# Performance work log

Hardware: AMD Instinct MI355X
Metric: run time of the kernel (lower is better)

The kernel has to match this reference:

```python
import jax, jax.numpy as jnp
import numpy as np

DIM = 1024
NUM_HEADS = 16
HEAD_DIM = DIM // NUM_HEADS
TGT_LEN = 4096


def setup_inputs() -> dict:
    key = jax.random.key(0)
    k1, k2, k3 = jax.random.split(key, 3)
    x = jax.random.normal(k1, (TGT_LEN, DIM), dtype=jnp.float32)
    W_in = jax.random.normal(k2, (3 * DIM, DIM), dtype=jnp.float32) * (DIM ** -0.5)
    W_out = jax.random.normal(k3, (DIM, DIM), dtype=jnp.float32) * (DIM ** -0.5)
    return {"x": x, "W_in": W_in, "W_out": W_out, "tgt_len": TGT_LEN}


def reference(x, W_in, W_out, tgt_len):
    # QKV projection (torch Linear: y = x @ W^T)
    qkv = x @ W_in.T  # [T, 3*dim]
    q, k, v = jnp.split(qkv, 3, axis=-1)
    # [T, dim] -> [H, T, hd]
    q = q.reshape(tgt_len, NUM_HEADS, HEAD_DIM).transpose(1, 0, 2)
    k = k.reshape(tgt_len, NUM_HEADS, HEAD_DIM).transpose(1, 0, 2)
    v = v.reshape(tgt_len, NUM_HEADS, HEAD_DIM).transpose(1, 0, 2)
    scaling = HEAD_DIM ** -0.5
    scores = jnp.einsum('htd,hsd->hts', q, k) * scaling  # [H, T, T]
    # joint softmax over the full (T, T) matrix per head (NOT row-wise)
    maxes = jnp.max(scores, axis=(1, 2), keepdims=True)
    x_exp = jnp.exp(scores - maxes)
    probs = x_exp / jnp.sum(x_exp, axis=(1, 2), keepdims=True)
    attn = jnp.einsum('hts,hsd->htd', probs, v)  # [H, T, hd]
    attn = attn.transpose(1, 0, 2).reshape(tgt_len, DIM)
    return attn @ W_out.T
```

## Files before the change

kernel.cpp:

```cpp
#include <hip/hip_runtime.h>

#define TLEN 4096
#define DIM 1024
#define NHEAD 16
#define HDIM 64
#define QKV_COLS (3 * DIM)
#define QSCALE 0.1803368801111244f
#define NCHUNK 2
#define SCHUNK (TLEN / NCHUNK)
#define TB 256

typedef __attribute__((ext_vector_type(8))) short short8;
typedef __attribute__((ext_vector_type(4))) float f32x4;

struct alignas(8) s4 { short v[4]; };

__device__ float g_Lsum[NHEAD];
__device__ float g_recipL[NHEAD];

__global__ void zeroL() {
    if (threadIdx.x < NHEAD) g_Lsum[threadIdx.x] = 0.0f;
}
__global__ void recipL() {
    if (threadIdx.x < NHEAD) g_recipL[threadIdx.x] = 1.0f / g_Lsum[threadIdx.x];
}

__device__ __forceinline__ unsigned bf16_rtne_bits(float x) {
    unsigned u = __float_as_uint(x);
    return (u + 0x7fffu + ((u >> 16) & 1u)) >> 16;
}

__device__ __forceinline__ void cp16(const short* g, short* l) {
    __builtin_amdgcn_global_load_lds(
        (const __attribute__((address_space(1))) unsigned int*)g,
        (__attribute__((address_space(3))) unsigned int*)l,
        16, 0, 0);
}

__device__ __forceinline__ short8 mk8(unsigned a, unsigned b, unsigned c, unsigned d) {
    union { unsigned u[4]; short8 s; } t;
    t.u[0] = a; t.u[1] = b; t.u[2] = c; t.u[3] = d;
    return t.s;
}

__global__ __launch_bounds__(256) void conv_bf16(
    const float* __restrict__ src, short* __restrict__ dst, int n4)
{
    int i = blockIdx.x * 256 + threadIdx.x;
    if (i < n4) {
        float4 v = ((const float4*)src)[i];
        s4 o;
        o.v[0] = (short)bf16_rtne_bits(v.x);
        o.v[1] = (short)bf16_rtne_bits(v.y);
        o.v[2] = (short)bf16_rtne_bits(v.z);
        o.v[3] = (short)bf16_rtne_bits(v.w);
        ((s4*)dst)[i] = o;
    }
}

__global__ __launch_bounds__(256) void conv_wout(
    const float* __restrict__ src, short* __restrict__ dst)
{
    int i = blockIdx.x * 256 + threadIdx.x;
    float s = g_recipL[(i & 255) >> 4];
    float4 v = ((const float4*)src)[i];
    s4 o;
    o.v[0] = (short)bf16_rtne_bits(v.x * s);
    o.v[1] = (short)bf16_rtne_bits(v.y * s);
    o.v[2] = (short)bf16_rtne_bits(v.z * s);
    o.v[3] = (short)bf16_rtne_bits(v.w * s);
    ((s4*)dst)[i] = o;
}

__global__ __launch_bounds__(256) void combine(
    const short* __restrict__ p0, const short* __restrict__ p1,
    short* __restrict__ dst, int n4)
{
    int i = blockIdx.x * 256 + threadIdx.x;
    if (i < n4) {
        s4 a = ((const s4*)p0)[i];
        s4 b = ((const s4*)p1)[i];
        s4 o;
#pragma unroll
        for (int m = 0; m < 4; ++m) {
            float fa = __uint_as_float(((unsigned)(unsigned short)a.v[m]) << 16);
            float fb = __uint_as_float(((unsigned)(unsigned short)b.v[m]) << 16);
            o.v[m] = (short)bf16_rtne_bits(fa + fb);
        }
        ((s4*)dst)[i] = o;
    }
}

template <bool QKV_MODE>
__global__ __launch_bounds__(256) void gemm_bt(
    const short* __restrict__ A, const short* __restrict__ B,
    void* __restrict__ Cout, short* __restrict__ Vout, int M, int N, int K)
{
    __shared__ __align__(16) short As[128][32];
    __shared__ __align__(16) short Bs[128][32];
    const int tid  = threadIdx.x;
    const int wv   = tid >> 6, lane = tid & 63;
    const int fr   = lane & 15, quad = lane >> 4;
    const int wm   = (wv >> 1) * 64, wn = (wv & 1) * 64;
    const int m0 = blockIdx.x * 128, n0 = blockIdx.y * 128;

    f32x4 acc[4][4] = {};

    for (int k0 = 0; k0 < K; k0 += 32) {
        __syncthreads();
#pragma unroll
        for (int c = tid; c < 512; c += 256) {
            int row = c >> 2, col = (c & 3) * 8;
            cp16(A + (size_t)(m0 + row) * K + k0 + col, &As[row][col]);
            cp16(B + (size_t)(n0 + row) * K + k0 + col, &Bs[row][col]);
        }
        __syncthreads();

        short8 af[4], bfr[4];
#pragma unroll
        for (int i = 0; i < 4; ++i) {
            af[i]  = *(const short8*)&As[wm + i * 16 + fr][quad * 8];
            bfr[i] = *(const short8*)&Bs[wn + i * 16 + fr][quad * 8];
        }
#pragma unroll
        for (int i = 0; i < 4; ++i)
#pragma unroll
            for (int j = 0; j < 4; ++j)
                acc[i][j] = __builtin_amdgcn_mfma_f32_16x16x32_bf16(af[i], bfr[j], acc[i][j], 0, 0, 0);
    }

    if (QKV_MODE && n0 >= 2 * DIM) {
#pragma unroll
        for (int i = 0; i < 4; ++i)
#pragma unroll
            for (int j = 0; j < 4; ++j) {
                int n = n0 - 2 * DIM + wn + j * 16 + fr;
                int m = m0 + wm + i * 16 + quad * 4;
                unsigned u0 = bf16_rtne_bits(acc[i][j][0]);
                unsigned u1 = bf16_rtne_bits(acc[i][j][1]);
                unsigned u2 = bf16_rtne_bits(acc[i][j][2]);
                unsigned u3 = bf16_rtne_bits(acc[i][j][3]);
                uint2 pk;
                pk.x = u0 | (u1 << 16);
                pk.y = u2 | (u3 << 16);
                *(uint2*)(Vout + (size_t)n * TLEN + m) = pk;
            }
    } else if (QKV_MODE) {
        const float sc = (n0 < DIM) ? QSCALE : 1.0f;
#pragma unroll
        for (int i = 0; i < 4; ++i)
#pragma unroll
            for (int j = 0; j < 4; ++j)
#pragma unroll
                for (int r = 0; r < 4; ++r) {
                    size_t off = (size_t)(m0 + wm + i * 16 + quad * 4 + r) * N + n0 + wn + j * 16 + fr;
                    ((short*)Cout)[off] = (short)bf16_rtne_bits(acc[i][j][r] * sc);
                }
    } else {
#pragma unroll
        for (int i = 0; i < 4; ++i)
#pragma unroll
            for (int j = 0; j < 4; ++j)
#pragma unroll
                for (int r = 0; r < 4; ++r) {
                    size_t off = (size_t)(m0 + wm + i * 16 + quad * 4 + r) * N + n0 + wn + j * 16 + fr;
                    ((float*)Cout)[off] = acc[i][j][r];
                }
    }
}

__global__ __launch_bounds__(256, 2) void attn_mfma(
    const short* __restrict__ qkvb, const short* __restrict__ vtb,
    short* __restrict__ part)
{
    __shared__ __align__(16) short Ks[64][72];
    __shared__ __align__(16) short Vt[64][72];
    __shared__ float red[256];

    const int tid = threadIdx.x;
    const int t0 = blockIdx.x * TB;
    const int h  = blockIdx.y;
    const int chunk = blockIdx.z;
    const int srow = tid >> 2;
    const int sch  = (tid & 3) * 16;
    const int wv   = tid >> 6;
    const int lane = tid & 63;
    const int fr   = lane & 15;
    const int quad = lane >> 4;
    const int tb   = wv * 64;

    short8 qf[4][2];
#pragma unroll
    for (int jt = 0; jt < 4; ++jt) {
        const short* qsrc = qkvb + (size_t)(t0 + tb + jt * 16 + fr) * QKV_COLS + h * HDIM + quad * 8;
        qf[jt][0] = *(const short8*)qsrc;
        qf[jt][1] = *(const short8*)(qsrc + 32);
    }

    short8 ones;
#pragma unroll
    for (int m = 0; m < 8; ++m) ones[m] = (short)0x3F80;

    f32x4 oaccT[4][4] = {};
    f32x4 racc[4] = {};

    const int s_begin = chunk * SCHUNK;
    const short* kbase = qkvb + DIM + h * HDIM + sch;
    const short* vbase = vtb + (size_t)(h * HDIM + srow) * TLEN + sch;

    uint4 kA, kB, vA, vB;
    {
        const short* ks = kbase + (size_t)(s_begin + srow) * QKV_COLS;
        kA = *(const uint4*)ks;  kB = *(const uint4*)(ks + 8);
        const short* vs = vbase + s_begin;
        vA = *(const uint4*)vs;  vB = *(const uint4*)(vs + 8);
    }

    for (int it = 0; it < SCHUNK / 64; ++it) {
        *(uint4*)&Ks[srow][sch]     = kA;
        *(uint4*)&Ks[srow][sch + 8] = kB;
        *(uint4*)&Vt[srow][sch]     = vA;
        *(uint4*)&Vt[srow][sch + 8] = vB;
        __syncthreads();

        if (it + 1 < SCHUNK / 64) {
            const int s0n = s_begin + (it + 1) * 64;
            const short* ks = kbase + (size_t)(s0n + srow) * QKV_COLS;
            kA = *(const uint4*)ks;  kB = *(const uint4*)(ks + 8);
            const short* vs = vbase + s0n;
            vA = *(const uint4*)vs;  vB = *(const uint4*)(vs + 8);
        }

        short8 kf[4][2], vf[4][2];
#pragma unroll
        for (int i = 0; i < 4; ++i) {
            kf[i][0] = *(const short8*)&Ks[i * 16 + fr][quad * 8];
            kf[i][1] = *(const short8*)&Ks[i * 16 + fr][32 + quad * 8];
            vf[i][0] = *(const short8*)&Vt[i * 16 + fr][quad * 8];
            vf[i][1] = *(const short8*)&Vt[i * 16 + fr][32 + quad * 8];
        }

#pragma unroll
        for (int jt = 0; jt < 4; ++jt) {
            unsigned w0[4], w1[4];
#pragma unroll
            for (int i = 0; i < 4; ++i) {
                f32x4 acc = {};
                acc = __builtin_amdgcn_mfma_f32_16x16x32_bf16(kf[i][0], qf[jt][0], acc, 0, 0, 0);
                acc = __builtin_amdgcn_mfma_f32_16x16x32_bf16(kf[i][1], qf[jt][1], acc, 0, 0, 0);
                unsigned u0 = __float_as_uint(__builtin_amdgcn_exp2f(acc[0]));
                unsigned u1 = __float_as_uint(__builtin_amdgcn_exp2f(acc[1]));
                unsigned u2 = __float_as_uint(__builtin_amdgcn_exp2f(acc[2]));
                unsigned u3 = __float_as_uint(__builtin_amdgcn_exp2f(acc[3]));
                w0[i] = __builtin_amdgcn_perm(u1, u0, 0x07060302);
                w1[i] = __builtin_amdgcn_perm(u3, u2, 0x07060302);
            }
            auto A0 = __builtin_amdgcn_permlane32_swap(w0[0], w0[1], false, false);
            auto A2 = __builtin_amdgcn_permlane32_swap(w0[2], w0[3], false, false);
            auto B0 = __builtin_amdgcn_permlane32_swap(w1[0], w1[1], false, false);
            auto B2 = __builtin_amdgcn_permlane32_swap(w1[2], w1[3], false, false);
            auto O0 = __builtin_amdgcn_permlane16_swap(A0[0], A0[1], false, false);
            auto O2 = __builtin_amdgcn_permlane16_swap(A2[0], A2[1], false, false);
            auto P0 = __builtin_amdgcn_permlane16_swap(B0[0], B0[1], false, false);
            auto P2 = __builtin_amdgcn_permlane16_swap(B2[0], B2[1], false, false);
            short8 pb0 = mk8(O0[0], P0[0], O0[1], P0[1]);
            short8 pb1 = mk8(O2[0], P2[0], O2[1], P2[1]);

            racc[jt] = __builtin_amdgcn_mfma_f32_16x16x32_bf16(ones, pb0, racc[jt], 0, 0, 0);
            racc[jt] = __builtin_amdgcn_mfma_f32_16x16x32_bf16(ones, pb1, racc[jt], 0, 0, 0);

#pragma unroll
            for (int jd = 0; jd < 4; ++jd) {
                oaccT[jd][jt] = __builtin_amdgcn_mfma_f32_16x16x32_bf16(vf[jd][0], pb0, oaccT[jd][jt], 0, 0, 0);
                oaccT[jd][jt] = __builtin_amdgcn_mfma_f32_16x16x32_bf16(vf[jd][1], pb1, oaccT[jd][jt], 0, 0, 0);
            }
        }
        __syncthreads();
    }

    short* pc = part + (size_t)chunk * TLEN * DIM;
#pragma unroll
    for (int jt = 0; jt < 4; ++jt)
#pragma unroll
        for (int jd = 0; jd < 4; ++jd) {
            unsigned u0 = bf16_rtne_bits(oaccT[jd][jt][0]);
            unsigned u1 = bf16_rtne_bits(oaccT[jd][jt][1]);
            unsigned u2 = bf16_rtne_bits(oaccT[jd][jt][2]);
            unsigned u3 = bf16_rtne_bits(oaccT[jd][jt][3]);
            uint2 pk;
            pk.x = u0 | (u1 << 16);
            pk.y = u2 | (u3 << 16);
            *(uint2*)(pc + (size_t)(t0 + tb + jt * 16 + fr) * DIM + h * HDIM + jd * 16 + quad * 4) = pk;
        }

    red[tid] = (racc[0][0] + racc[1][0] + racc[2][0] + racc[3][0]) * 0.25f;
    __syncthreads();
    for (int off = 128; off > 0; off >>= 1) {
        if (tid < off) red[tid] += red[tid + off];
        __syncthreads();
    }
    if (tid == 0) atomicAdd(&g_Lsum[h], red[0]);
}

extern "C" void kernel_launch(void* const* d_in, const int* in_sizes, int n_in,
                              void* d_out, int out_size, void* d_ws, size_t ws_size,
                              hipStream_t stream)
{
    const float* x     = (const float*)d_in[0];
    const float* W_in  = (const float*)d_in[1];
    const float* W_out = (const float*)d_in[2];
    float* out = (float*)d_out;

    char* ws = (char*)d_ws;
    short* xb    = (short*)(ws);
    short* wib   = (short*)(ws + (8u << 20));
    short* wob   = (short*)(ws + (14u << 20));
    short* qkvb  = (short*)(ws + (16u << 20));
    short* vtb   = (short*)(ws + (40u << 20));
    short* part  = (short*)(ws + (48u << 20));
    short* attnb = xb;

    zeroL<<<1, 64, 0, stream>>>();

    conv_bf16<<<(TLEN * DIM / 4 + 255) / 256, 256, 0, stream>>>(x, xb, TLEN * DIM / 4);
    conv_bf16<<<(QKV_COLS * DIM / 4 + 255) / 256, 256, 0, stream>>>(W_in, wib, QKV_COLS * DIM / 4);

    gemm_bt<true><<<dim3(TLEN / 128, QKV_COLS / 128), 256, 0, stream>>>(
        xb, wib, qkvb, vtb, TLEN, QKV_COLS, DIM);

    attn_mfma<<<dim3(TLEN / TB, NHEAD, NCHUNK), 256, 0, stream>>>(qkvb, vtb, part);

    recipL<<<1, 64, 0, stream>>>();
    conv_wout<<<(DIM * DIM / 4 + 255) / 256, 256, 0, stream>>>(W_out, wob);

    combine<<<(TLEN * DIM / 4 + 255) / 256, 256, 0, stream>>>(
        part, part + (size_t)TLEN * DIM, attnb, TLEN * DIM / 4);

    gemm_bt<false><<<dim3(TLEN / 128, DIM / 128), 256, 0, stream>>>(
        attnb, wob, out, nullptr, TLEN, DIM, DIM);
}
```

Measured before the change: 220.4 us.

## Double-buffer K/V tiles in LDS and raise wave priority around MFMAs

The attention loop now uses two LDS buffers for K and V tiles. While computing on the current buffer, each iteration stores the next tile into the other buffer and issues global loads two tiles ahead, so one __syncthreads per iteration replaces two. s_setprio is raised around the PV MFMA block to favour matrix issue over other waves' memory and exp work. The extra buffers double LDS use, which may affect occupancy at two blocks per CU, and prefetched values stay live in registers for longer.

```diff
diff --git a/kernel.cpp b/kernel.cpp
--- a/kernel.cpp
+++ b/kernel.cpp
@@ -9,6 +9,7 @@
 #define NCHUNK 2
 #define SCHUNK (TLEN / NCHUNK)
 #define TB 256
+#define NIT (SCHUNK / 64)
 
 typedef __attribute__((ext_vector_type(8))) short short8;
 typedef __attribute__((ext_vector_type(4))) float f32x4;
@@ -173,8 +174,8 @@
     const short* __restrict__ qkvb, const short* __restrict__ vtb,
     short* __restrict__ part)
 {
-    __shared__ __align__(16) short Ks[64][72];
-    __shared__ __align__(16) short Vt[64][72];
+    __shared__ __align__(16) short Ks[2][64][72];
+    __shared__ __align__(16) short Vt[2][64][72];
     __shared__ float red[256];
 
     const int tid = threadIdx.x;
@@ -215,16 +216,28 @@
         const short* vs = vbase + s_begin;
         vA = *(const uint4*)vs;  vB = *(const uint4*)(vs + 8);
     }
-
-    for (int it = 0; it < SCHUNK / 64; ++it) {
-        *(uint4*)&Ks[srow][sch]     = kA;
-        *(uint4*)&Ks[srow][sch + 8] = kB;
-        *(uint4*)&Vt[srow][sch]     = vA;
-        *(uint4*)&Vt[srow][sch + 8] = vB;
-        __syncthreads();
-
-        if (it + 1 < SCHUNK / 64) {
-            const int s0n = s_begin + (it + 1) * 64;
+    *(uint4*)&Ks[0][srow][sch]     = kA;
+    *(uint4*)&Ks[0][srow][sch + 8] = kB;
+    *(uint4*)&Vt[0][srow][sch]     = vA;
+    *(uint4*)&Vt[0][srow][sch + 8] = vB;
+    {
+        const short* ks = kbase + (size_t)(s_begin + 64 + srow) * QKV_COLS;
+        kA = *(const uint4*)ks;  kB = *(const uint4*)(ks + 8);
+        const short* vs = vbase + s_begin + 64;
+        vA = *(const uint4*)vs;  vB = *(const uint4*)(vs + 8);
+    }
+    __syncthreads();
+
+    auto step = [&](short (*KsC)[72], short (*VtC)[72],
+                    short (*KsN)[72], short (*VtN)[72], int it) {
+        if (it + 1 < NIT) {
+            *(uint4*)&KsN[srow][sch]     = kA;
+            *(uint4*)&KsN[srow][sch + 8] = kB;
+            *(uint4*)&VtN[srow][sch]     = vA;
+            *(uint4*)&VtN[srow][sch + 8] = vB;
+        }
+        if (it + 2 < NIT) {
+            const int s0n = s_begin + (it + 2) * 64;
             const short* ks = kbase + (size_t)(s0n + srow) * QKV_COLS;
             kA = *(const uint4*)ks;  kB = *(const uint4*)(ks + 8);
             const short* vs = vbase + s0n;
@@ -234,10 +247,10 @@
         short8 kf[4][2], vf[4][2];
 #pragma unroll
         for (int i = 0; i < 4; ++i) {
-            kf[i][0] = *(const short8*)&Ks[i * 16 + fr][quad * 8];
-            kf[i][1] = *(const short8*)&Ks[i * 16 + fr][32 + quad * 8];
-            vf[i][0] = *(const short8*)&Vt[i * 16 + fr][quad * 8];
-            vf[i][1] = *(const short8*)&Vt[i * 16 + fr][32 + quad * 8];
+            kf[i][0] = *(const short8*)&KsC[i * 16 + fr][quad * 8];
+            kf[i][1] = *(const short8*)&KsC[i * 16 + fr][32 + quad * 8];
+            vf[i][0] = *(const short8*)&VtC[i * 16 + fr][quad * 8];
+            vf[i][1] = *(const short8*)&VtC[i * 16 + fr][32 + quad * 8];
         }
 
 #pragma unroll
@@ -266,6 +279,7 @@
             short8 pb0 = mk8(O0[0], P0[0], O0[1], P0[1]);
             short8 pb1 = mk8(O2[0], P2[0], O2[1], P2[1]);
 
+            __builtin_amdgcn_s_setprio(1);
             racc[jt] = __builtin_amdgcn_mfma_f32_16x16x32_bf16(ones, pb0, racc[jt], 0, 0, 0);
             racc[jt] = __builtin_amdgcn_mfma_f32_16x16x32_bf16(ones, pb1, racc[jt], 0, 0, 0);
 
@@ -274,8 +288,14 @@
                 oaccT[jd][jt] = __builtin_amdgcn_mfma_f32_16x16x32_bf16(vf[jd][0], pb0, oaccT[jd][jt], 0, 0, 0);
                 oaccT[jd][jt] = __builtin_amdgcn_mfma_f32_16x16x32_bf16(vf[jd][1], pb1, oaccT[jd][jt], 0, 0, 0);
             }
+            __builtin_amdgcn_s_setprio(0);
         }
         __syncthreads();
+    };
+
+    for (int it = 0; it < NIT; it += 2) {
+        step(Ks[0], Vt[0], Ks[1], Vt[1], it);
+        step(Ks[1], Vt[1], Ks[0], Vt[0], it + 1);
     }
 
     short* pc = part + (size_t)chunk * TLEN * DIM;
```

New measurement: 221.4 us. Within noise of the previous version (+0.4%).
